# Performance work log

Measured on AMD Instinct MI355X. Metric: run time of the kernel, lower is better.

## Reference

```python
import jax, jax.numpy as jnp
import numpy as np

N = 100000
E = 3200000
IN_DIM = 768
HID = 128
NUM_CLASSES = 7


def gcn_conv(x, W, b, src, dst, n):
    """PyG GCNConv: h = D^-1/2 (A+I) D^-1/2 (x W) + b, symmetric normalization."""
    h = x @ W  # [n, out]
    loop = jnp.arange(n, dtype=src.dtype)
    s = jnp.concatenate([src, loop])  # sources (messages flow src -> dst)
    d = jnp.concatenate([dst, loop])
    deg = jax.ops.segment_sum(jnp.ones(s.shape[0], dtype=h.dtype), d, num_segments=n)
    dinv = jnp.where(deg > 0, jax.lax.rsqrt(deg), 0.0)
    norm = dinv[s] * dinv[d]  # [E+n]
    msgs = h[s] * norm[:, None]
    out = jax.ops.segment_sum(msgs, d, num_segments=n)
    return out + b


def setup_inputs() -> dict:
    key = jax.random.key(0)
    ks = jax.random.split(key, 8)
    x = jax.random.normal(ks[0], (N, IN_DIM), dtype=jnp.float32)
    edge_index = jax.random.randint(ks[1], (2, E), 0, N, dtype=jnp.int32)
    W1 = jax.random.normal(ks[2], (IN_DIM, HID), dtype=jnp.float32) / np.sqrt(IN_DIM)
    b1 = jnp.zeros((HID,), dtype=jnp.float32)
    W2 = jax.random.normal(ks[3], (HID, HID), dtype=jnp.float32) / np.sqrt(HID)
    b2 = jnp.zeros((HID,), dtype=jnp.float32)
    Wc = jax.random.normal(ks[4], (HID, NUM_CLASSES), dtype=jnp.float32) / np.sqrt(HID)
    bc = jnp.zeros((NUM_CLASSES,), dtype=jnp.float32)
    return {"x": x, "edge_index": edge_index, "W1": W1, "b1": b1,
            "W2": W2, "b2": b2, "Wc": Wc, "bc": bc}


def reference(x, edge_index, W1, b1, W2, b2, Wc, bc):
    src, dst = edge_index[0], edge_index[1]
    n = x.shape[0]
    h = jax.nn.relu(gcn_conv(x, W1, b1, src, dst, n))
    h = jax.nn.relu(gcn_conv(h, W2, b2, src, dst, n))
    logits = h @ Wc + bc
    return logits
```

## Files before the change

kernel.cpp:

```cpp
#include <hip/hip_runtime.h>
#include <hip/hip_bf16.h>

#define IN_DIM 768
#define HID 128
#define NC 7

typedef __attribute__((ext_vector_type(8))) short bf16x8;
typedef __attribute__((ext_vector_type(4))) float f32x4;

__device__ __forceinline__ ushort f2bf(float f) {
  uint u = __float_as_uint(f);
  u += 0x7fffu + ((u >> 16) & 1u);
  return (ushort)(u >> 16);
}
__device__ __forceinline__ float lof(uint v) { return __uint_as_float(v << 16); }
__device__ __forceinline__ float hif(uint v) { return __uint_as_float(v & 0xffff0000u); }


__global__ __launch_bounds__(256) void k_count(const int* __restrict__ dst,
                                               int* __restrict__ cnt,
                                               int* __restrict__ pos, int E) {
  int e0 = (blockIdx.x * 256 + threadIdx.x) * 4;
  if (e0 + 4 <= E) {
    int4 d = *(const int4*)&dst[e0];
    int4 p;
    p.x = atomicAdd(&cnt[d.x], 1);
    p.y = atomicAdd(&cnt[d.y], 1);
    p.z = atomicAdd(&cnt[d.z], 1);
    p.w = atomicAdd(&cnt[d.w], 1);
    *(int4*)&pos[e0] = p;
  } else {
    for (int e = e0; e < E; ++e) pos[e] = atomicAdd(&cnt[dst[e]], 1);
  }
}

__device__ __forceinline__ int pad4(int c) { return (c + 3) & ~3; }

__global__ void k_scan_partial(const int* __restrict__ cnt, int* __restrict__ partials, int N) {
  __shared__ int sm[256];
  int b = blockIdx.x, t = threadIdx.x;
  int base = b * 1024 + t * 4;
  int s = 0;
  #pragma unroll
  for (int j = 0; j < 4; ++j) if (base + j < N) s += pad4(cnt[base + j]);
  sm[t] = s;
  __syncthreads();
  for (int off = 128; off > 0; off >>= 1) {
    if (t < off) sm[t] += sm[t + off];
    __syncthreads();
  }
  if (t == 0) partials[b] = sm[0];
}

__global__ void k_scan_combine(int* __restrict__ partials, int* __restrict__ rowptr,
                               int nch, int N) {
  __shared__ int sm[128];
  int t = threadIdx.x;
  int v0 = (t < nch) ? partials[t] : 0;
  sm[t] = v0;
  __syncthreads();
  for (int off = 1; off < 128; off <<= 1) {
    int add = (t >= off) ? sm[t - off] : 0;
    __syncthreads();
    sm[t] += add;
    __syncthreads();
  }
  if (t < nch) partials[t] = sm[t] - v0;
  if (t == 0) rowptr[N] = sm[127];
}

__global__ void k_scan_final(const int* __restrict__ cnt, const int* __restrict__ chunkoff,
                             int* __restrict__ rowptr, int N) {
  __shared__ int sm[256];
  int b = blockIdx.x, t = threadIdx.x;
  int base = b * 1024 + t * 4;
  int v[4]; int s = 0;
  #pragma unroll
  for (int j = 0; j < 4; ++j) { v[j] = (base + j < N) ? pad4(cnt[base + j]) : 0; s += v[j]; }
  sm[t] = s;
  __syncthreads();
  for (int off = 1; off < 256; off <<= 1) {
    int add = (t >= off) ? sm[t - off] : 0;
    __syncthreads();
    sm[t] += add;
    __syncthreads();
  }
  int excl = sm[t] - s;
  int run = chunkoff[b] + excl;
  #pragma unroll
  for (int j = 0; j < 4; ++j) {
    if (base + j < N) rowptr[base + j] = run;
    run += v[j];
  }
}

__global__ void k_dinv(const int* __restrict__ cnt, float* __restrict__ dinv, int N) {
  int n = blockIdx.x * 256 + threadIdx.x;
  if (n <= N) dinv[n] = (n < N) ? rsqrtf((float)(cnt[n] + 1)) : 0.f;
}

__global__ void k_fill(int* __restrict__ p, int val, int total) {
  int i = (blockIdx.x * 256 + threadIdx.x) * 4;
  if (i + 4 <= total) {
    *(int4*)&p[i] = make_int4(val, val, val, val);
  } else {
    for (; i < total; ++i) p[i] = val;
  }
}

__global__ __launch_bounds__(256)
void k_scatter(const int* __restrict__ src, const int* __restrict__ dst,
               const int* __restrict__ pos, const int* __restrict__ rowptr,
               int* __restrict__ srcs, int E) {
  int e0 = (blockIdx.x * 256 + threadIdx.x) * 8;
  if (e0 + 8 <= E) {
    int s[8], d[8], p[8];
    *(int4*)&s[0] = *(const int4*)&src[e0];
    *(int4*)&s[4] = *(const int4*)&src[e0 + 4];
    *(int4*)&d[0] = *(const int4*)&dst[e0];
    *(int4*)&d[4] = *(const int4*)&dst[e0 + 4];
    *(int4*)&p[0] = *(const int4*)&pos[e0];
    *(int4*)&p[4] = *(const int4*)&pos[e0 + 4];
    int rp[8];
    #pragma unroll
    for (int j = 0; j < 8; ++j) rp[j] = rowptr[d[j]];
    #pragma unroll
    for (int j = 0; j < 8; ++j) srcs[rp[j] + p[j]] = s[j];
  } else {
    for (int e = e0; e < E; ++e) srcs[rowptr[dst[e]] + pos[e]] = src[e];
  }
}

__global__ void k_convW(const float* __restrict__ W, ushort* __restrict__ WT, int K) {
  int i = blockIdx.x * 256 + threadIdx.x;
  if (i >= K * HID) return;
  int k = i >> 7, c = i & 127;
  WT[c * K + k] = f2bf(W[i]);
}

template<int K, bool AF32>
__global__ __launch_bounds__(256)
void gemm_bf(const void* __restrict__ Ap, const ushort* __restrict__ WT,
             ushort* __restrict__ Hout, const int N) {
  __shared__ ushort lA[2][128 * 64];
  __shared__ ushort lB[2][128 * 64];
  const int tid = threadIdx.x;
  const int lane = tid & 63;
  const int wid = tid >> 6;
  const int wm = wid >> 1, wn = wid & 1;
  const int row0 = blockIdx.x * 128;
  const int lr = lane & 15;
  const int lk8 = lane >> 4;
  const ushort* Abf = (const ushort*)Ap;
  const float*  Af  = (const float*)Ap;

  auto stageB = [&](int buf, int k0) {
    #pragma unroll
    for (int j = 0; j < 4; ++j) {
      int i = j * 256 + tid;
      int r = i >> 3;
      int c = ((i & 7) ^ (r & 7)) * 8;
      __builtin_amdgcn_global_load_lds((const uint*)(WT + (size_t)r * K + k0 + c),
                                       (uint*)&lB[buf][i * 8], 16, 0, 0);
    }
  };
  auto stageA_lds = [&](int buf, int k0) {
    #pragma unroll
    for (int j = 0; j < 4; ++j) {
      int i = j * 256 + tid;
      int r = i >> 3;
      int c = ((i & 7) ^ (r & 7)) * 8;
      int ga = row0 + r; ga = ga < N ? ga : N - 1;
      __builtin_amdgcn_global_load_lds((const uint*)(Abf + (size_t)ga * K + k0 + c),
                                       (uint*)&lA[buf][i * 8], 16, 0, 0);
    }
  };

  float4 fa[8];
  auto loadA = [&](int k0) {
    #pragma unroll
    for (int j = 0; j < 4; ++j) {
      int i = j * 256 + tid;
      int r = i >> 3;
      int c = (i & 7) * 8;
      int ga = row0 + r; ga = ga < N ? ga : N - 1;
      const float* p = Af + (size_t)ga * K + k0 + c;
      fa[j * 2]     = *(const float4*)p;
      fa[j * 2 + 1] = *(const float4*)(p + 4);
    }
  };
  auto writeA = [&](int buf) {
    #pragma unroll
    for (int j = 0; j < 4; ++j) {
      int i = j * 256 + tid;
      int r = i >> 3;
      int slot = (i & 7) ^ (r & 7);
      float4 u = fa[j * 2], v = fa[j * 2 + 1];
      uint4 pk;
      pk.x = (uint)f2bf(u.x) | ((uint)f2bf(u.y) << 16);
      pk.y = (uint)f2bf(u.z) | ((uint)f2bf(u.w) << 16);
      pk.z = (uint)f2bf(v.x) | ((uint)f2bf(v.y) << 16);
      pk.w = (uint)f2bf(v.z) | ((uint)f2bf(v.w) << 16);
      *(uint4*)&lA[buf][r * 64 + slot * 8] = pk;
    }
  };

  f32x4 acc[4][4];
  #pragma unroll
  for (int m = 0; m < 4; ++m)
    #pragma unroll
    for (int n = 0; n < 4; ++n)
      acc[m][n] = (f32x4){0.f, 0.f, 0.f, 0.f};

  constexpr int NT = K / 64;
  if constexpr (AF32) {
    loadA(0); stageB(0, 0); writeA(0);
  } else {
    stageA_lds(0, 0); stageB(0, 0);
  }
  __syncthreads();

  for (int t = 0; t < NT; ++t) {
    const int cur = t & 1;
    if (t + 1 < NT) {
      if constexpr (AF32) loadA((t + 1) * 64);
      else stageA_lds(cur ^ 1, (t + 1) * 64);
      stageB(cur ^ 1, (t + 1) * 64);
    }
    #pragma unroll
    for (int kk = 0; kk < 2; ++kk) {
      bf16x8 av[4], bv[4];
      #pragma unroll
      for (int m = 0; m < 4; ++m) {
        int R = wm * 64 + m * 16 + lr;
        int slot = (kk * 4 + lk8) ^ (R & 7);
        av[m] = *(const bf16x8*)&lA[cur][R * 64 + slot * 8];
      }
      #pragma unroll
      for (int n = 0; n < 4; ++n) {
        int C = wn * 64 + n * 16 + lr;
        int slot = (kk * 4 + lk8) ^ (C & 7);
        bv[n] = *(const bf16x8*)&lB[cur][C * 64 + slot * 8];
      }
      #pragma unroll
      for (int m = 0; m < 4; ++m)
        #pragma unroll
        for (int n = 0; n < 4; ++n)
          acc[m][n] = __builtin_amdgcn_mfma_f32_16x16x32_bf16(av[m], bv[n], acc[m][n], 0, 0, 0);
    }
    if (t + 1 < NT) {
      if constexpr (AF32) writeA(cur ^ 1);
    }
    __syncthreads();
  }

  #pragma unroll
  for (int m = 0; m < 4; ++m) {
    #pragma unroll
    for (int i = 0; i < 4; ++i) {
      int row = row0 + wm * 64 + m * 16 + (lane >> 4) * 4 + i;
      if (row < N) {
        #pragma unroll
        for (int n = 0; n < 4; ++n) {
          int col = wn * 64 + n * 16 + lr;
          Hout[(size_t)row * HID + col] = f2bf(acc[m][n][i]);
        }
      }
    }
  }
}


#define GATHER1(s, w, h, idx) \
  int s = idx; float w = dinv[s]; uint h = Hu[(size_t)s * 64 + lane];

__device__ __forceinline__ void agg_b16(const uint* __restrict__ Hu,
                                        const int* __restrict__ srcs,
                                        const float* __restrict__ dinv,
                                        int i, int lane, float& a0, float& a1) {
  int4 sa = *(const int4*)&srcs[i];
  int4 sb = *(const int4*)&srcs[i + 4];
  int4 sc = *(const int4*)&srcs[i + 8];
  int4 sd = *(const int4*)&srcs[i + 12];
  GATHER1(s0, w0, h0, sa.x) GATHER1(s1, w1, h1, sa.y)
  GATHER1(s2, w2, h2, sa.z) GATHER1(s3, w3, h3, sa.w)
  GATHER1(s4, w4, h4, sb.x) GATHER1(s5, w5, h5, sb.y)
  GATHER1(s6, w6, h6, sb.z) GATHER1(s7, w7, h7, sb.w)
  GATHER1(s8, w8, h8, sc.x) GATHER1(s9, w9, h9, sc.y)
  GATHER1(sA, wA, hA, sc.z) GATHER1(sB, wB, hB, sc.w)
  GATHER1(sC, wC, hC, sd.x) GATHER1(sD, wD, hD, sd.y)
  GATHER1(sE, wE, hE, sd.z) GATHER1(sF, wF, hF, sd.w)
  __builtin_amdgcn_sched_barrier(0);
  a0 += w0 * lof(h0); a1 += w0 * hif(h0);
  a0 += w1 * lof(h1); a1 += w1 * hif(h1);
  a0 += w2 * lof(h2); a1 += w2 * hif(h2);
  a0 += w3 * lof(h3); a1 += w3 * hif(h3);
  a0 += w4 * lof(h4); a1 += w4 * hif(h4);
  a0 += w5 * lof(h5); a1 += w5 * hif(h5);
  a0 += w6 * lof(h6); a1 += w6 * hif(h6);
  a0 += w7 * lof(h7); a1 += w7 * hif(h7);
  a0 += w8 * lof(h8); a1 += w8 * hif(h8);
  a0 += w9 * lof(h9); a1 += w9 * hif(h9);
  a0 += wA * lof(hA); a1 += wA * hif(hA);
  a0 += wB * lof(hB); a1 += wB * hif(hB);
  a0 += wC * lof(hC); a1 += wC * hif(hC);
  a0 += wD * lof(hD); a1 += wD * hif(hD);
  a0 += wE * lof(hE); a1 += wE * hif(hE);
  a0 += wF * lof(hF); a1 += wF * hif(hF);
}

__device__ __forceinline__ void agg_b4(const uint* __restrict__ Hu,
                                       const int* __restrict__ srcs,
                                       const float* __restrict__ dinv,
                                       int i, int lane, float& a0, float& a1) {
  int4 sa = *(const int4*)&srcs[i];
  GATHER1(s0, w0, h0, sa.x) GATHER1(s1, w1, h1, sa.y)
  GATHER1(s2, w2, h2, sa.z) GATHER1(s3, w3, h3, sa.w)
  __builtin_amdgcn_sched_barrier(0);
  a0 += w0 * lof(h0); a1 += w0 * hif(h0);
  a0 += w1 * lof(h1); a1 += w1 * hif(h1);
  a0 += w2 * lof(h2); a1 += w2 * hif(h2);
  a0 += w3 * lof(h3); a1 += w3 * hif(h3);
}

__global__ __launch_bounds__(256)
void k_agg(const uint* __restrict__ Hu, const int* __restrict__ srcs,
           const int* __restrict__ rowptr, const float* __restrict__ dinv,
           const float* __restrict__ bias, uint* __restrict__ Ou, int N) {
  int w = (blockIdx.x * 256 + threadIdx.x) >> 6;
  if (w >= N) return;
  int lane = threadIdx.x & 63;
  int start = rowptr[w], end = rowptr[w + 1];
  float di = dinv[w];
  uint hv = Hu[(size_t)w * 64 + lane];
  float a0 = di * lof(hv);
  float a1 = di * hif(hv);
  int i = start;
  for (; i + 16 <= end; i += 16) agg_b16(Hu, srcs, dinv, i, lane, a0, a1);
  for (; i < end; i += 4)        agg_b4(Hu, srcs, dinv, i, lane, a0, a1);
  float2 bb = ((const float2*)bias)[lane];
  a0 = fmaxf(di * a0 + bb.x, 0.f);
  a1 = fmaxf(di * a1 + bb.y, 0.f);
  Ou[(size_t)w * 64 + lane] = (uint)f2bf(a0) | ((uint)f2bf(a1) << 16);
}

__global__ __launch_bounds__(256)
void k_agg_final(const uint* __restrict__ Hu, const int* __restrict__ srcs,
                 const int* __restrict__ rowptr, const float* __restrict__ dinv,
                 const float* __restrict__ bias, const float* __restrict__ Wc,
                 const float* __restrict__ bc, float* __restrict__ out, int N) {
  int w = (blockIdx.x * 256 + threadIdx.x) >> 6;
  if (w >= N) return;
  int lane = threadIdx.x & 63;
  int start = rowptr[w], end = rowptr[w + 1];
  float di = dinv[w];
  uint hv = Hu[(size_t)w * 64 + lane];
  float a0 = di * lof(hv);
  float a1 = di * hif(hv);
  int i = start;
  for (; i + 16 <= end; i += 16) agg_b16(Hu, srcs, dinv, i, lane, a0, a1);
  for (; i < end; i += 4)        agg_b4(Hu, srcs, dinv, i, lane, a0, a1);
  float2 bb = ((const float2*)bias)[lane];
  a0 = fmaxf(di * a0 + bb.x, 0.f);
  a1 = fmaxf(di * a1 + bb.y, 0.f);
  const float* w0 = &Wc[(2 * lane) * NC];
  #pragma unroll
  for (int c = 0; c < NC; ++c) {
    float s = a0 * w0[c] + a1 * w0[NC + c];
    #pragma unroll
    for (int off = 32; off > 0; off >>= 1) s += __shfl_xor(s, off, 64);
    if (lane == 0) out[(size_t)w * NC + c] = s + bc[c];
  }
}

extern "C" void kernel_launch(void* const* d_in, const int* in_sizes, int n_in,
                              void* d_out, int out_size, void* d_ws, size_t ws_size,
                              hipStream_t stream) {
  const float* x  = (const float*)d_in[0];
  const int*   ei = (const int*)d_in[1];
  const float* W1 = (const float*)d_in[2];
  const float* b1 = (const float*)d_in[3];
  const float* W2 = (const float*)d_in[4];
  const float* b2 = (const float*)d_in[5];
  const float* Wc = (const float*)d_in[6];
  const float* bc = (const float*)d_in[7];
  float* out = (float*)d_out;

  const int N = in_sizes[0] / IN_DIM;
  const int E = in_sizes[1] / 2;
  const int* src = ei;
  const int* dst = ei + E;
  const int CSRCAP = E + 3 * N + 64;

  char* ws = (char*)d_ws;
  size_t off = 0;
  auto alloc = [&](size_t bytes) -> void* {
    off = (off + 255) & ~(size_t)255;
    void* p = ws + off;
    off += bytes;
    return p;
  };
  ushort* H0     = (ushort*)alloc((size_t)(N + 1) * HID * 2);
  ushort* H1     = (ushort*)alloc((size_t)(N + 1) * HID * 2);
  int*    srcs   = (int*)alloc((size_t)CSRCAP * 4);
  int*    cnt    = (int*)alloc((size_t)N * 4);
  int*    pos    = (int*)alloc((size_t)E * 4);
  int*    rowptr = (int*)alloc((size_t)(N + 1) * 4);
  float*  dinv   = (float*)alloc((size_t)(N + 1) * 4);
  int*    partials = (int*)alloc(512);
  ushort* W1T    = (ushort*)alloc((size_t)IN_DIM * HID * 2);
  ushort* W2T    = (ushort*)alloc((size_t)HID * HID * 2);

  hipMemsetAsync(cnt, 0, (size_t)N * 4, stream);

  k_convW<<<(IN_DIM * HID + 255) / 256, 256, 0, stream>>>(W1, W1T, IN_DIM);
  k_convW<<<(HID * HID + 255) / 256, 256, 0, stream>>>(W2, W2T, HID);

  k_count<<<(E + 1023) / 1024, 256, 0, stream>>>(dst, cnt, pos, E);
  int nch = (N + 1023) >> 10;
  k_scan_partial<<<nch, 256, 0, stream>>>(cnt, partials, N);
  k_scan_combine<<<1, 128, 0, stream>>>(partials, rowptr, nch, N);
  k_scan_final<<<nch, 256, 0, stream>>>(cnt, partials, rowptr, N);
  k_dinv<<<(N + 256) / 256, 256, 0, stream>>>(cnt, dinv, N);
  k_fill<<<(CSRCAP + 1023) / 1024, 256, 0, stream>>>(srcs, N, CSRCAP);
  k_scatter<<<(E + 2047) / 2048, 256, 0, stream>>>(src, dst, pos, rowptr, srcs, E);

  gemm_bf<IN_DIM, true><<<(N + 127) / 128, 256, 0, stream>>>(x, W1T, H0, N);
  k_agg<<<(N + 3) / 4, 256, 0, stream>>>((const uint*)H0, srcs, rowptr, dinv, b1, (uint*)H1, N);
  gemm_bf<HID, false><<<(N + 127) / 128, 256, 0, stream>>>(H1, W2T, H0, N);
  k_agg_final<<<(N + 3) / 4, 256, 0, stream>>>((const uint*)H0, srcs, rowptr, dinv, b2,
                                               Wc, bc, out, N);
}
```

Before: 585.2 us.

## Prescale GEMM outputs by dinv and split gather across half-waves

The source-side dinv scaling is folded into the GEMM epilogues, so aggregation no longer gathers dinv per edge. The aggregation kernels now let each half-wave handle alternate edges with uint2 loads and combine the halves with a shuffle, which halves the instruction count per edge. Padding edges point at a zeroed row N of H0. The first-layer GEMM is rewritten to load fp32 A straight into registers per wave, convert it with v_cvt_pk_bf16_f32 and stage only W in LDS, which drops the LDS round trip for A but puts more register pressure on 64-row tiles.

```diff
diff --git a/kernel.cpp b/kernel.cpp
--- a/kernel.cpp
+++ b/kernel.cpp
@@ -15,6 +15,11 @@
 }
 __device__ __forceinline__ float lof(uint v) { return __uint_as_float(v << 16); }
 __device__ __forceinline__ float hif(uint v) { return __uint_as_float(v & 0xffff0000u); }
+__device__ __forceinline__ uint cvtpk(float lo, float hi) {
+  uint r;
+  asm("v_cvt_pk_bf16_f32 %0, %1, %2" : "=v"(r) : "v"(lo), "v"(hi));
+  return r;
+}
 
 
 __global__ __launch_bounds__(256) void k_count(const int* __restrict__ dst,
@@ -96,7 +101,7 @@
 
 __global__ void k_dinv(const int* __restrict__ cnt, float* __restrict__ dinv, int N) {
   int n = blockIdx.x * 256 + threadIdx.x;
-  if (n <= N) dinv[n] = (n < N) ? rsqrtf((float)(cnt[n] + 1)) : 0.f;
+  if (n < N) dinv[n] = rsqrtf((float)(cnt[n] + 1));
 }
 
 __global__ void k_fill(int* __restrict__ p, int val, int total) {
@@ -138,10 +143,90 @@
   WT[c * K + k] = f2bf(W[i]);
 }
 
-template<int K, bool AF32>
 __global__ __launch_bounds__(256)
-void gemm_bf(const void* __restrict__ Ap, const ushort* __restrict__ WT,
-             ushort* __restrict__ Hout, const int N) {
+void k_gemm1(const float* __restrict__ A, const ushort* __restrict__ WT,
+             const float* __restrict__ dinv, ushort* __restrict__ G, const int N) {
+  __shared__ ushort lB[2][128 * 64];
+  const int tid = threadIdx.x;
+  const int lane = tid & 63;
+  const int wid = tid >> 6;
+  const int lr = lane & 15, lq = lane >> 4;
+  const int r0 = blockIdx.x * 64 + wid * 16;
+  int arow = r0 + lr; if (arow > N - 1) arow = N - 1;
+  const float* Ap = A + (size_t)arow * IN_DIM + lq * 8;
+
+  auto stageB = [&](int buf, int k0) {
+    #pragma unroll
+    for (int j = 0; j < 4; ++j) {
+      int i = j * 256 + tid;
+      int r = i >> 3;
+      int c = ((i & 7) ^ (r & 7)) * 8;
+      __builtin_amdgcn_global_load_lds((const uint*)(WT + (size_t)r * IN_DIM + k0 + c),
+                                       (uint*)&lB[buf][i * 8], 16, 0, 0);
+    }
+  };
+
+  float4 fa[4];
+  auto loadA = [&](int k0) {
+    const float* p = Ap + k0;
+    fa[0] = *(const float4*)p;
+    fa[1] = *(const float4*)(p + 4);
+    fa[2] = *(const float4*)(p + 32);
+    fa[3] = *(const float4*)(p + 36);
+  };
+
+  f32x4 acc[8];
+  #pragma unroll
+  for (int n = 0; n < 8; ++n) acc[n] = (f32x4){0.f, 0.f, 0.f, 0.f};
+
+  loadA(0);
+  stageB(0, 0);
+  __syncthreads();
+
+  constexpr int NT = IN_DIM / 64;
+  for (int t = 0; t < NT; ++t) {
+    const int cur = t & 1;
+    bf16x8 av[2];
+    {
+      uint* u = (uint*)&av[0];
+      u[0] = cvtpk(fa[0].x, fa[0].y); u[1] = cvtpk(fa[0].z, fa[0].w);
+      u[2] = cvtpk(fa[1].x, fa[1].y); u[3] = cvtpk(fa[1].z, fa[1].w);
+      u[4] = cvtpk(fa[2].x, fa[2].y); u[5] = cvtpk(fa[2].z, fa[2].w);
+      u[6] = cvtpk(fa[3].x, fa[3].y); u[7] = cvtpk(fa[3].z, fa[3].w);
+    }
+    if (t + 1 < NT) { loadA((t + 1) * 64); stageB(cur ^ 1, (t + 1) * 64); }
+    #pragma unroll
+    for (int kk = 0; kk < 2; ++kk) {
+      #pragma unroll
+      for (int n = 0; n < 8; ++n) {
+        int C = n * 16 + lr;
+        int slot = (kk * 4 + lq) ^ (C & 7);
+        bf16x8 bv = *(const bf16x8*)&lB[cur][C * 64 + slot * 8];
+        acc[n] = __builtin_amdgcn_mfma_f32_16x16x32_bf16(av[kk], bv, acc[n], 0, 0, 0);
+      }
+    }
+    __syncthreads();
+  }
+
+  float dv[4];
+  #pragma unroll
+  for (int i = 0; i < 4; ++i) {
+    int row = r0 + lq * 4 + i;
+    dv[i] = (row < N) ? dinv[row] : 0.f;
+  }
+  #pragma unroll
+  for (int n = 0; n < 8; ++n) {
+    #pragma unroll
+    for (int i = 0; i < 4; ++i) {
+      int row = r0 + lq * 4 + i;
+      if (row < N) G[(size_t)row * HID + n * 16 + lr] = f2bf(dv[i] * acc[n][i]);
+    }
+  }
+}
+
+__global__ __launch_bounds__(256)
+void k_gemm2(const ushort* __restrict__ A, const ushort* __restrict__ WT,
+             const float* __restrict__ dinv, ushort* __restrict__ G, const int N) {
   __shared__ ushort lA[2][128 * 64];
   __shared__ ushort lB[2][128 * 64];
   const int tid = threadIdx.x;
@@ -151,57 +236,19 @@
   const int row0 = blockIdx.x * 128;
   const int lr = lane & 15;
   const int lk8 = lane >> 4;
-  const ushort* Abf = (const ushort*)Ap;
-  const float*  Af  = (const float*)Ap;
-
-  auto stageB = [&](int buf, int k0) {
-    #pragma unroll
-    for (int j = 0; j < 4; ++j) {
-      int i = j * 256 + tid;
-      int r = i >> 3;
-      int c = ((i & 7) ^ (r & 7)) * 8;
-      __builtin_amdgcn_global_load_lds((const uint*)(WT + (size_t)r * K + k0 + c),
-                                       (uint*)&lB[buf][i * 8], 16, 0, 0);
-    }
-  };
-  auto stageA_lds = [&](int buf, int k0) {
+  constexpr int K = HID;
+
+  auto stage = [&](int buf, int k0) {
     #pragma unroll
     for (int j = 0; j < 4; ++j) {
       int i = j * 256 + tid;
       int r = i >> 3;
       int c = ((i & 7) ^ (r & 7)) * 8;
       int ga = row0 + r; ga = ga < N ? ga : N - 1;
-      __builtin_amdgcn_global_load_lds((const uint*)(Abf + (size_t)ga * K + k0 + c),
+      __builtin_amdgcn_global_load_lds((const uint*)(A + (size_t)ga * K + k0 + c),
                                        (uint*)&lA[buf][i * 8], 16, 0, 0);
-    }
-  };
-
-  float4 fa[8];
-  auto loadA = [&](int k0) {
-    #pragma unroll
-    for (int j = 0; j < 4; ++j) {
-      int i = j * 256 + tid;
-      int r = i >> 3;
-      int c = (i & 7) * 8;
-      int ga = row0 + r; ga = ga < N ? ga : N - 1;
-      const float* p = Af + (size_t)ga * K + k0 + c;
-      fa[j * 2]     = *(const float4*)p;
-      fa[j * 2 + 1] = *(const float4*)(p + 4);
-    }
-  };
-  auto writeA = [&](int buf) {
-    #pragma unroll
-    for (int j = 0; j < 4; ++j) {
-      int i = j * 256 + tid;
-      int r = i >> 3;
-      int slot = (i & 7) ^ (r & 7);
-      float4 u = fa[j * 2], v = fa[j * 2 + 1];
-      uint4 pk;
-      pk.x = (uint)f2bf(u.x) | ((uint)f2bf(u.y) << 16);
-      pk.y = (uint)f2bf(u.z) | ((uint)f2bf(u.w) << 16);
-      pk.z = (uint)f2bf(v.x) | ((uint)f2bf(v.y) << 16);
-      pk.w = (uint)f2bf(v.z) | ((uint)f2bf(v.w) << 16);
-      *(uint4*)&lA[buf][r * 64 + slot * 8] = pk;
+      __builtin_amdgcn_global_load_lds((const uint*)(WT + (size_t)r * K + k0 + c),
+                                       (uint*)&lB[buf][i * 8], 16, 0, 0);
     }
   };
 
@@ -213,20 +260,12 @@
       acc[m][n] = (f32x4){0.f, 0.f, 0.f, 0.f};
 
   constexpr int NT = K / 64;
-  if constexpr (AF32) {
-    loadA(0); stageB(0, 0); writeA(0);
-  } else {
-    stageA_lds(0, 0); stageB(0, 0);
-  }
+  stage(0, 0);
   __syncthreads();
 
   for (int t = 0; t < NT; ++t) {
     const int cur = t & 1;
-    if (t + 1 < NT) {
-      if constexpr (AF32) loadA((t + 1) * 64);
-      else stageA_lds(cur ^ 1, (t + 1) * 64);
-      stageB(cur ^ 1, (t + 1) * 64);
-    }
+    if (t + 1 < NT) stage(cur ^ 1, (t + 1) * 64);
     #pragma unroll
     for (int kk = 0; kk < 2; ++kk) {
       bf16x8 av[4], bv[4];
@@ -248,9 +287,6 @@
         for (int n = 0; n < 4; ++n)
           acc[m][n] = __builtin_amdgcn_mfma_f32_16x16x32_bf16(av[m], bv[n], acc[m][n], 0, 0, 0);
     }
-    if (t + 1 < NT) {
-      if constexpr (AF32) writeA(cur ^ 1);
-    }
     __syncthreads();
   }
 
@@ -260,10 +296,11 @@
     for (int i = 0; i < 4; ++i) {
       int row = row0 + wm * 64 + m * 16 + (lane >> 4) * 4 + i;
       if (row < N) {
+        float dv = dinv[row];
         #pragma unroll
         for (int n = 0; n < 4; ++n) {
           int col = wn * 64 + n * 16 + lr;
-          Hout[(size_t)row * HID + col] = f2bf(acc[m][n][i]);
+          G[(size_t)row * HID + col] = f2bf(dv * acc[m][n][i]);
         }
       }
     }
@@ -271,104 +308,95 @@
 }
 
 
-#define GATHER1(s, w, h, idx) \
-  int s = idx; float w = dinv[s]; uint h = Hu[(size_t)s * 64 + lane];
-
-__device__ __forceinline__ void agg_b16(const uint* __restrict__ Hu,
-                                        const int* __restrict__ srcs,
-                                        const float* __restrict__ dinv,
-                                        int i, int lane, float& a0, float& a1) {
-  int4 sa = *(const int4*)&srcs[i];
-  int4 sb = *(const int4*)&srcs[i + 4];
-  int4 sc = *(const int4*)&srcs[i + 8];
-  int4 sd = *(const int4*)&srcs[i + 12];
-  GATHER1(s0, w0, h0, sa.x) GATHER1(s1, w1, h1, sa.y)
-  GATHER1(s2, w2, h2, sa.z) GATHER1(s3, w3, h3, sa.w)
-  GATHER1(s4, w4, h4, sb.x) GATHER1(s5, w5, h5, sb.y)
-  GATHER1(s6, w6, h6, sb.z) GATHER1(s7, w7, h7, sb.w)
-  GATHER1(s8, w8, h8, sc.x) GATHER1(s9, w9, h9, sc.y)
-  GATHER1(sA, wA, hA, sc.z) GATHER1(sB, wB, hB, sc.w)
-  GATHER1(sC, wC, hC, sd.x) GATHER1(sD, wD, hD, sd.y)
-  GATHER1(sE, wE, hE, sd.z) GATHER1(sF, wF, hF, sd.w)
-  __builtin_amdgcn_sched_barrier(0);
-  a0 += w0 * lof(h0); a1 += w0 * hif(h0);
-  a0 += w1 * lof(h1); a1 += w1 * hif(h1);
-  a0 += w2 * lof(h2); a1 += w2 * hif(h2);
-  a0 += w3 * lof(h3); a1 += w3 * hif(h3);
-  a0 += w4 * lof(h4); a1 += w4 * hif(h4);
-  a0 += w5 * lof(h5); a1 += w5 * hif(h5);
-  a0 += w6 * lof(h6); a1 += w6 * hif(h6);
-  a0 += w7 * lof(h7); a1 += w7 * hif(h7);
-  a0 += w8 * lof(h8); a1 += w8 * hif(h8);
-  a0 += w9 * lof(h9); a1 += w9 * hif(h9);
-  a0 += wA * lof(hA); a1 += wA * hif(hA);
-  a0 += wB * lof(hB); a1 += wB * hif(hB);
-  a0 += wC * lof(hC); a1 += wC * hif(hC);
-  a0 += wD * lof(hD); a1 += wD * hif(hD);
-  a0 += wE * lof(hE); a1 += wE * hif(hE);
-  a0 += wF * lof(hF); a1 += wF * hif(hF);
-}
-
-__device__ __forceinline__ void agg_b4(const uint* __restrict__ Hu,
-                                       const int* __restrict__ srcs,
-                                       const float* __restrict__ dinv,
-                                       int i, int lane, float& a0, float& a1) {
-  int4 sa = *(const int4*)&srcs[i];
-  GATHER1(s0, w0, h0, sa.x) GATHER1(s1, w1, h1, sa.y)
-  GATHER1(s2, w2, h2, sa.z) GATHER1(s3, w3, h3, sa.w)
-  __builtin_amdgcn_sched_barrier(0);
-  a0 += w0 * lof(h0); a1 += w0 * hif(h0);
-  a0 += w1 * lof(h1); a1 += w1 * hif(h1);
-  a0 += w2 * lof(h2); a1 += w2 * hif(h2);
-  a0 += w3 * lof(h3); a1 += w3 * hif(h3);
+#define PLOAD(vv, sl, sh) uint2 vv = Gm[(size_t)(half ? (sh) : (sl)) * 32 + l32];
+#define PACC(vv) { a0 += lof(vv.x); a1 += hif(vv.x); a2 += lof(vv.y); a3 += hif(vv.y); }
+
+__device__ __forceinline__ void agg_core(const uint2* __restrict__ Gm,
+                                         const int* __restrict__ srcs,
+                                         int start, int end, int half, int l32,
+                                         float& a0, float& a1, float& a2, float& a3) {
+  int i = start;
+  for (; i + 16 <= end; i += 16) {
+    int4 sa = *(const int4*)&srcs[i];
+    int4 sb = *(const int4*)&srcs[i + 4];
+    int4 sc = *(const int4*)&srcs[i + 8];
+    int4 sd = *(const int4*)&srcs[i + 12];
+    PLOAD(v0, sa.x, sa.y) PLOAD(v1, sa.z, sa.w)
+    PLOAD(v2, sb.x, sb.y) PLOAD(v3, sb.z, sb.w)
+    PLOAD(v4, sc.x, sc.y) PLOAD(v5, sc.z, sc.w)
+    PLOAD(v6, sd.x, sd.y) PLOAD(v7, sd.z, sd.w)
+    __builtin_amdgcn_sched_barrier(0);
+    PACC(v0) PACC(v1) PACC(v2) PACC(v3)
+    PACC(v4) PACC(v5) PACC(v6) PACC(v7)
+  }
+  for (; i < end; i += 4) {
+    int4 sa = *(const int4*)&srcs[i];
+    PLOAD(v0, sa.x, sa.y) PLOAD(v1, sa.z, sa.w)
+    __builtin_amdgcn_sched_barrier(0);
+    PACC(v0) PACC(v1)
+  }
 }
 
 __global__ __launch_bounds__(256)
-void k_agg(const uint* __restrict__ Hu, const int* __restrict__ srcs,
+void k_agg(const uint2* __restrict__ Gm, const int* __restrict__ srcs,
            const int* __restrict__ rowptr, const float* __restrict__ dinv,
-           const float* __restrict__ bias, uint* __restrict__ Ou, int N) {
+           const float* __restrict__ bias, uint2* __restrict__ Ou, int N) {
   int w = (blockIdx.x * 256 + threadIdx.x) >> 6;
   if (w >= N) return;
   int lane = threadIdx.x & 63;
+  int half = lane >> 5, l32 = lane & 31;
   int start = rowptr[w], end = rowptr[w + 1];
   float di = dinv[w];
-  uint hv = Hu[(size_t)w * 64 + lane];
-  float a0 = di * lof(hv);
-  float a1 = di * hif(hv);
-  int i = start;
-  for (; i + 16 <= end; i += 16) agg_b16(Hu, srcs, dinv, i, lane, a0, a1);
-  for (; i < end; i += 4)        agg_b4(Hu, srcs, dinv, i, lane, a0, a1);
-  float2 bb = ((const float2*)bias)[lane];
-  a0 = fmaxf(di * a0 + bb.x, 0.f);
-  a1 = fmaxf(di * a1 + bb.y, 0.f);
-  Ou[(size_t)w * 64 + lane] = (uint)f2bf(a0) | ((uint)f2bf(a1) << 16);
+  float a0, a1, a2, a3;
+  uint2 sv = Gm[(size_t)w * 32 + l32];
+  if (half == 0) { a0 = lof(sv.x); a1 = hif(sv.x); a2 = lof(sv.y); a3 = hif(sv.y); }
+  else           { a0 = a1 = a2 = a3 = 0.f; }
+  agg_core(Gm, srcs, start, end, half, l32, a0, a1, a2, a3);
+  a0 += __shfl_xor(a0, 32); a1 += __shfl_xor(a1, 32);
+  a2 += __shfl_xor(a2, 32); a3 += __shfl_xor(a3, 32);
+  if (lane < 32) {
+    float4 bb = ((const float4*)bias)[l32];
+    a0 = fmaxf(fmaf(di, a0, bb.x), 0.f);
+    a1 = fmaxf(fmaf(di, a1, bb.y), 0.f);
+    a2 = fmaxf(fmaf(di, a2, bb.z), 0.f);
+    a3 = fmaxf(fmaf(di, a3, bb.w), 0.f);
+    uint2 o;
+    o.x = (uint)f2bf(a0) | ((uint)f2bf(a1) << 16);
+    o.y = (uint)f2bf(a2) | ((uint)f2bf(a3) << 16);
+    Ou[(size_t)w * 32 + l32] = o;
+  }
 }
 
 __global__ __launch_bounds__(256)
-void k_agg_final(const uint* __restrict__ Hu, const int* __restrict__ srcs,
+void k_agg_final(const uint2* __restrict__ Gm, const int* __restrict__ srcs,
                  const int* __restrict__ rowptr, const float* __restrict__ dinv,
                  const float* __restrict__ bias, const float* __restrict__ Wc,
                  const float* __restrict__ bc, float* __restrict__ out, int N) {
   int w = (blockIdx.x * 256 + threadIdx.x) >> 6;
   if (w >= N) return;
   int lane = threadIdx.x & 63;
+  int half = lane >> 5, l32 = lane & 31;
   int start = rowptr[w], end = rowptr[w + 1];
   float di = dinv[w];
-  uint hv = Hu[(size_t)w * 64 + lane];
-  float a0 = di * lof(hv);
-  float a1 = di * hif(hv);
-  int i = start;
-  for (; i + 16 <= end; i += 16) agg_b16(Hu, srcs, dinv, i, lane, a0, a1);
-  for (; i < end; i += 4)        agg_b4(Hu, srcs, dinv, i, lane, a0, a1);
-  float2 bb = ((const float2*)bias)[lane];
-  a0 = fmaxf(di * a0 + bb.x, 0.f);
-  a1 = fmaxf(di * a1 + bb.y, 0.f);
-  const float* w0 = &Wc[(2 * lane) * NC];
+  float a0, a1, a2, a3;
+  uint2 sv = Gm[(size_t)w * 32 + l32];
+  if (half == 0) { a0 = lof(sv.x); a1 = hif(sv.x); a2 = lof(sv.y); a3 = hif(sv.y); }
+  else           { a0 = a1 = a2 = a3 = 0.f; }
+  agg_core(Gm, srcs, start, end, half, l32, a0, a1, a2, a3);
+  a0 += __shfl_xor(a0, 32); a1 += __shfl_xor(a1, 32);
+  a2 += __shfl_xor(a2, 32); a3 += __shfl_xor(a3, 32);
+  float4 bb = ((const float4*)bias)[l32];
+  a0 = fmaxf(fmaf(di, a0, bb.x), 0.f);
+  a1 = fmaxf(fmaf(di, a1, bb.y), 0.f);
+  a2 = fmaxf(fmaf(di, a2, bb.z), 0.f);
+  a3 = fmaxf(fmaf(di, a3, bb.w), 0.f);
+  const float* w0 = &Wc[(4 * l32) * NC];
   #pragma unroll
   for (int c = 0; c < NC; ++c) {
-    float s = a0 * w0[c] + a1 * w0[NC + c];
-    #pragma unroll
-    for (int off = 32; off > 0; off >>= 1) s += __shfl_xor(s, off, 64);
+    float s = a0 * w0[c] + a1 * w0[NC + c] + a2 * w0[2 * NC + c] + a3 * w0[3 * NC + c];
+    s += __shfl_xor(s, 16); s += __shfl_xor(s, 8);
+    s += __shfl_xor(s, 4);  s += __shfl_xor(s, 2);
+    s += __shfl_xor(s, 1);
     if (lane == 0) out[(size_t)w * NC + c] = s + bc[c];
   }
 }
@@ -406,12 +434,13 @@
   int*    cnt    = (int*)alloc((size_t)N * 4);
   int*    pos    = (int*)alloc((size_t)E * 4);
   int*    rowptr = (int*)alloc((size_t)(N + 1) * 4);
-  float*  dinv   = (float*)alloc((size_t)(N + 1) * 4);
+  float*  dinv   = (float*)alloc((size_t)N * 4);
   int*    partials = (int*)alloc(512);
   ushort* W1T    = (ushort*)alloc((size_t)IN_DIM * HID * 2);
   ushort* W2T    = (ushort*)alloc((size_t)HID * HID * 2);
 
   hipMemsetAsync(cnt, 0, (size_t)N * 4, stream);
+  hipMemsetAsync(H0 + (size_t)N * HID, 0, HID * 2, stream);
 
   k_convW<<<(IN_DIM * HID + 255) / 256, 256, 0, stream>>>(W1, W1T, IN_DIM);
   k_convW<<<(HID * HID + 255) / 256, 256, 0, stream>>>(W2, W2T, HID);
@@ -421,13 +450,14 @@
   k_scan_partial<<<nch, 256, 0, stream>>>(cnt, partials, N);
   k_scan_combine<<<1, 128, 0, stream>>>(partials, rowptr, nch, N);
   k_scan_final<<<nch, 256, 0, stream>>>(cnt, partials, rowptr, N);
-  k_dinv<<<(N + 256) / 256, 256, 0, stream>>>(cnt, dinv, N);
+  k_dinv<<<(N + 255) / 256, 256, 0, stream>>>(cnt, dinv, N);
   k_fill<<<(CSRCAP + 1023) / 1024, 256, 0, stream>>>(srcs, N, CSRCAP);
   k_scatter<<<(E + 2047) / 2048, 256, 0, stream>>>(src, dst, pos, rowptr, srcs, E);
 
-  gemm_bf<IN_DIM, true><<<(N + 127) / 128, 256, 0, stream>>>(x, W1T, H0, N);
-  k_agg<<<(N + 3) / 4, 256, 0, stream>>>((const uint*)H0, srcs, rowptr, dinv, b1, (uint*)H1, N);
-  gemm_bf<HID, false><<<(N + 127) / 128, 256, 0, stream>>>(H1, W2T, H0, N);
-  k_agg_final<<<(N + 3) / 4, 256, 0, stream>>>((const uint*)H0, srcs, rowptr, dinv, b2,
+  k_gemm1<<<(N + 63) / 64, 256, 0, stream>>>(x, W1T, dinv, H0, N);
+  k_agg<<<(N + 3) / 4, 256, 0, stream>>>((const uint2*)H0, srcs, rowptr, dinv, b1,
+                                         (uint2*)H1, N);
+  k_gemm2<<<(N + 127) / 128, 256, 0, stream>>>(H1, W2T, dinv, H0, N);
+  k_agg_final<<<(N + 3) / 4, 256, 0, stream>>>((const uint2*)H0, srcs, rowptr, dinv, b2,
                                                Wc, bc, out, N);
 }
```

After: 689.3 us. 1.18x slower.
